# Kernel tuning notes

Measured on AMD Instinct MI355X. Metric: run time of the kernel, lower is better.

Reference implementation:

```python
import jax, jax.numpy as jnp
import numpy as np

D_MODEL = 1024
N_HEADS = 16
HEAD_DIM = D_MODEL // N_HEADS
ALPHA = 1.5
SEQ, BATCH = 4096, 8


def reduced_sparsemax(z, alpha):
    # projection of z/alpha onto the simplex along the last axis
    zs = z / alpha
    z_sorted = -jnp.sort(-zs, axis=-1)          # descending sort
    z_cumsum = jnp.cumsum(z_sorted, axis=-1)
    d = zs.shape[-1]
    r = jnp.arange(1, d + 1, dtype=zs.dtype)
    support = (z_sorted - (z_cumsum - 1.0) / r) > 0
    k = jnp.sum(support, axis=-1, keepdims=True)
    k_safe = jnp.clip(k, 1, None)
    tau_sum = jnp.take_along_axis(z_cumsum, k_safe - 1, axis=-1)
    tau = (tau_sum - 1.0) / k_safe.astype(zs.dtype)
    return jnp.clip(zs - tau, 0.0, None)


def setup_inputs() -> dict:
    key = jax.random.key(0)
    ks = jax.random.split(key, 11)
    s = 0.02
    return {
        "query": jax.random.normal(ks[0], (SEQ, BATCH, D_MODEL), jnp.float32),
        "key":   jax.random.normal(ks[1], (SEQ, BATCH, D_MODEL), jnp.float32),
        "value": jax.random.normal(ks[2], (SEQ, BATCH, D_MODEL), jnp.float32),
        "Wq": jax.random.normal(ks[3], (D_MODEL, D_MODEL), jnp.float32) * s,
        "bq": jnp.zeros((D_MODEL,), jnp.float32),
        "Wk": jax.random.normal(ks[4], (D_MODEL, D_MODEL), jnp.float32) * s,
        "bk": jnp.zeros((D_MODEL,), jnp.float32),
        "Wv": jax.random.normal(ks[5], (D_MODEL, D_MODEL), jnp.float32) * s,
        "bv": jnp.zeros((D_MODEL,), jnp.float32),
        "Wo": jax.random.normal(ks[6], (D_MODEL, D_MODEL), jnp.float32) * s,
        "bo": jnp.zeros((D_MODEL,), jnp.float32),
    }


def reference(query, key, value, Wq, bq, Wk, bk, Wv, bv, Wo, bo):
    A, B, D = query.shape  # (seq, batch, d_model) per the torch code's indexing
    H, hd = N_HEADS, HEAD_DIM
    Q = query @ Wq.T + bq
    K = key @ Wk.T + bk
    V = value @ Wv.T + bv
    # view(A, B, H, hd).transpose(0, 1) -> (B, A, H, hd)
    Q = jnp.swapaxes(Q.reshape(A, B, H, hd), 0, 1)
    K = jnp.swapaxes(K.reshape(A, B, H, hd), 0, 1)
    V = jnp.swapaxes(V.reshape(A, B, H, hd), 0, 1)
    # NOTE: faithful to the original code, attention is across HEADS:
    # scores shape (B, A, H, H)
    scores = jnp.einsum('bahd,bagd->bahg', Q, K) / jnp.sqrt(
        jnp.asarray(hd, jnp.float32))
    attn = reduced_sparsemax(scores, ALPHA)
    attn_out = jnp.einsum('bahg,bagd->bahd', attn, V)  # (B, A, H, hd)
    # transpose(1,2).view(B, -1, D): (B, H, A, hd) flattened to (B, A, D)
    attn_out = jnp.swapaxes(attn_out, 1, 2).reshape(B, -1, D)
    out = attn_out @ Wo.T + bo           # (B, A, D)
    return jnp.swapaxes(out, 0, 1)       # (A, B, D)
```

## Files before the change

### kernel.cpp

```cpp
#include <hip/hip_runtime.h>
#include <hip/hip_bf16.h>
#include <stdint.h>

typedef __bf16 bf16_t;
typedef __bf16 bf16x4 __attribute__((ext_vector_type(4)));
typedef __bf16 bf16x8 __attribute__((ext_vector_type(8)));
typedef float  f32x4  __attribute__((ext_vector_type(4)));

#define AS_G __attribute__((address_space(1)))
#define AS_L __attribute__((address_space(3)))

__global__ void cast_f32_bf16(const float* __restrict__ src, bf16_t* __restrict__ dst) {
    int i = blockIdx.x * 256 + threadIdx.x;
    float4 v = ((const float4*)src)[i];
    bf16x4 o;
    o.x = (bf16_t)v.x; o.y = (bf16_t)v.y; o.z = (bf16_t)v.z; o.w = (bf16_t)v.w;
    ((bf16x4*)dst)[i] = o;
}

template<int OUT_BF16>
__global__ __launch_bounds__(512, 2)
void gemm_bt_kernel(const bf16_t* __restrict__ A,
                    const bf16_t* __restrict__ Bt,
                    const float* __restrict__ bias,
                    void* __restrict__ Cout,
                    int M, int N, int K) {
    __shared__ bf16_t smem[4][2][256 * 32];

    const int tid  = threadIdx.x;
    const int wave = tid >> 6, lane = tid & 63;
    const int quad = lane >> 4, r16 = lane & 15;
    const int wr = wave >> 2, wc = wave & 3;

    const int nbx = N >> 8;
    const int cpx = gridDim.x >> 3;
    const int swz = (blockIdx.x & 7) * cpx + (blockIdx.x >> 3);
    const int m0 = (swz / nbx) << 8;
    const int n0 = (swz % nbx) << 8;

    const int c0 = tid, c1 = 512 + tid;
    const int r0 = c0 >> 2, cc0 = c0 & 3;
    const int r1 = c1 >> 2, cc1 = c1 & 3;
    const int s0 = (r0 & 3) ^ ((r0 >> 2) & 3);
    const int s1 = (r1 & 3) ^ ((r1 >> 2) & 3);
    const bf16_t* gA0 = A  + (size_t)(m0 + r0) * K + ((cc0 ^ s0) << 3);
    const bf16_t* gA1 = A  + (size_t)(m0 + r1) * K + ((cc1 ^ s1) << 3);
    const bf16_t* gB0 = Bt + (size_t)(n0 + r0) * K + ((cc0 ^ s0) << 3);
    const bf16_t* gB1 = Bt + (size_t)(n0 + r1) * K + ((cc1 ^ s1) << 3);

#define STAGE(bufi, kt) do {                                                                    \
        const int _ko = (kt) << 5;                                                              \
        __builtin_amdgcn_global_load_lds((AS_G void*)(gA0 + _ko), (AS_L void*)(&smem[bufi][0][c0 * 8]), 16, 0, 0); \
        __builtin_amdgcn_global_load_lds((AS_G void*)(gA1 + _ko), (AS_L void*)(&smem[bufi][0][c1 * 8]), 16, 0, 0); \
        __builtin_amdgcn_global_load_lds((AS_G void*)(gB0 + _ko), (AS_L void*)(&smem[bufi][1][c0 * 8]), 16, 0, 0); \
        __builtin_amdgcn_global_load_lds((AS_G void*)(gB1 + _ko), (AS_L void*)(&smem[bufi][1][c1 * 8]), 16, 0, 0); \
    } while (0)

    f32x4 acc[8][4] = {};
    const int NT = K >> 5;

    STAGE(0, 0); STAGE(1, 1); STAGE(2, 2);

    const int swzc = quad ^ (r16 & 3) ^ ((r16 >> 2) & 3);
    const int aoff = ((wr * 128 + r16) << 5) + (swzc << 3);
    const int boff = ((wc * 64  + r16) << 5) + (swzc << 3);

    for (int t = 0; t < NT; ++t) {
        asm volatile("s_waitcnt vmcnt(8)\n\ts_barrier" ::: "memory");

        if (t + 3 < NT) STAGE((t + 3) & 3, t + 3);

        const bf16_t* pA = &smem[t & 3][0][0];
        const bf16_t* pB = &smem[t & 3][1][0];
        bf16x8 aF[8], bF[4];
#pragma unroll
        for (int i = 0; i < 8; ++i) aF[i] = *(const bf16x8*)(pA + aoff + i * 512);
#pragma unroll
        for (int i = 0; i < 4; ++i) bF[i] = *(const bf16x8*)(pB + boff + i * 512);

        __builtin_amdgcn_s_setprio(1);
#pragma unroll
        for (int tm = 0; tm < 8; ++tm)
#pragma unroll
            for (int tn = 0; tn < 4; ++tn)
                acc[tm][tn] = __builtin_amdgcn_mfma_f32_16x16x32_bf16(aF[tm], bF[tn], acc[tm][tn], 0, 0, 0);
        __builtin_amdgcn_s_setprio(0);
    }
#undef STAGE

    float bv[4];
#pragma unroll
    for (int tn = 0; tn < 4; ++tn) bv[tn] = bias[n0 + wc * 64 + tn * 16 + r16];

#pragma unroll
    for (int tm = 0; tm < 8; ++tm) {
#pragma unroll
        for (int r = 0; r < 4; ++r) {
            const int m = m0 + wr * 128 + tm * 16 + quad * 4 + r;
#pragma unroll
            for (int tn = 0; tn < 4; ++tn) {
                const int n = n0 + wc * 64 + tn * 16 + r16;
                const float v = acc[tm][tn][r] + bv[tn];
                if (OUT_BF16) ((bf16_t*)Cout)[(size_t)m * N + n] = (bf16_t)v;
                else          ((float*)Cout)[(size_t)m * N + n]  = v;
            }
        }
    }
}

__global__ void attn_kernel(const bf16_t* __restrict__ Q, const bf16_t* __restrict__ K,
                            const bf16_t* __restrict__ V, bf16_t* __restrict__ M2) {
    __shared__ float zs_s[4][16][17];
    __shared__ float tau_s[4][16];
    const int wave = threadIdx.x >> 6, lane = threadIdx.x & 63;
    const int quad = lane >> 4, g16 = lane & 15;
    const int p = blockIdx.x * 4 + wave;
    const int a = p >> 3, b = p & 7;
    const bf16_t* q = Q + (size_t)p * 1024;
    const bf16_t* k = K + (size_t)p * 1024;
    const bf16_t* v = V + (size_t)p * 1024;

    bf16x8 qa0 = *(const bf16x8*)(q + g16 * 64 + quad * 8);
    bf16x8 qa1 = *(const bf16x8*)(q + g16 * 64 + 32 + quad * 8);
    bf16x8 ka0 = *(const bf16x8*)(k + g16 * 64 + quad * 8);
    bf16x8 ka1 = *(const bf16x8*)(k + g16 * 64 + 32 + quad * 8);
    f32x4 sc = {0.f, 0.f, 0.f, 0.f};
    sc = __builtin_amdgcn_mfma_f32_16x16x32_bf16(qa0, ka0, sc, 0, 0, 0);
    sc = __builtin_amdgcn_mfma_f32_16x16x32_bf16(qa1, ka1, sc, 0, 0, 0);

    const float inv = 1.0f / 12.0f;
#pragma unroll
    for (int r = 0; r < 4; ++r) zs_s[wave][quad * 4 + r][g16] = sc[r] * inv;
    __syncthreads();

    if (lane < 16) {
        float z[16];
#pragma unroll
        for (int j = 0; j < 16; ++j) z[j] = zs_s[wave][lane][j];
#pragma unroll
        for (int kk = 2; kk <= 16; kk <<= 1) {
#pragma unroll
            for (int j = kk >> 1; j > 0; j >>= 1) {
#pragma unroll
                for (int i = 0; i < 16; ++i) {
                    int ixj = i ^ j;
                    if (ixj > i) {
                        bool desc = ((i & kk) == 0);
                        float zi = z[i], zj = z[ixj];
                        bool sw = desc ? (zi < zj) : (zi > zj);
                        z[i]   = sw ? zj : zi;
                        z[ixj] = sw ? zi : zj;
                    }
                }
            }
        }
        float cum = 0.f, csel = 0.f;
        int ksel = 1;
#pragma unroll
        for (int j = 0; j < 16; ++j) {
            cum += z[j];
            bool sup = z[j] * (float)(j + 1) > (cum - 1.0f);
            ksel = sup ? (j + 1) : ksel;
            csel = sup ? cum : csel;
        }
        tau_s[wave][lane] = (csel - 1.0f) / (float)ksel;
    }
    __syncthreads();

#pragma unroll
    for (int r = 0; r < 4; ++r) {
        float av = sc[r] * inv - tau_s[wave][quad * 4 + r];
        zs_s[wave][quad * 4 + r][g16] = av > 0.f ? av : 0.f;
    }
    __syncthreads();

    bf16x8 aP;
#pragma unroll
    for (int j = 0; j < 8; ++j) {
        float f = (quad < 2) ? zs_s[wave][g16][quad * 8 + j] : 0.f;
        aP[j] = (bf16_t)f;
    }
#pragma unroll
    for (int c = 0; c < 4; ++c) {
        bf16x8 bV;
#pragma unroll
        for (int j = 0; j < 8; ++j) {
            int g = quad * 8 + j;
            bV[j] = (quad < 2) ? v[g * 64 + c * 16 + g16] : (bf16_t)0.f;
        }
        f32x4 oc = {0.f, 0.f, 0.f, 0.f};
        oc = __builtin_amdgcn_mfma_f32_16x16x32_bf16(aP, bV, oc, 0, 0, 0);
#pragma unroll
        for (int r = 0; r < 4; ++r) {
            int h = quad * 4 + r;
            int e = c * 16 + g16;
            int rr = (h << 8) + (a >> 4);
            int c2 = ((a & 15) << 6) + e;
            M2[((size_t)(rr * 8 + b)) * 1024 + c2] = (bf16_t)oc[r];
        }
    }
}

extern "C" void kernel_launch(void* const* d_in, const int* in_sizes, int n_in,
                              void* d_out, int out_size, void* d_ws, size_t ws_size,
                              hipStream_t stream) {
    (void)in_sizes; (void)n_in; (void)out_size; (void)ws_size;
    const float* query = (const float*)d_in[0];
    const float* key   = (const float*)d_in[1];
    const float* value = (const float*)d_in[2];
    const float* Wq = (const float*)d_in[3];
    const float* bq = (const float*)d_in[4];
    const float* Wk = (const float*)d_in[5];
    const float* bk = (const float*)d_in[6];
    const float* Wv = (const float*)d_in[7];
    const float* bv = (const float*)d_in[8];
    const float* Wo = (const float*)d_in[9];
    const float* bo = (const float*)d_in[10];

    const int M = 32768, D = 1024;
    const size_t MD = (size_t)M * D;

    uint8_t* ws = (uint8_t*)d_ws;
    bf16_t* abuf = (bf16_t*)ws;
    bf16_t* Qb   = (bf16_t*)(ws + MD * 2);
    bf16_t* Kb   = Qb + MD;
    bf16_t* Vb   = Kb + MD;
    bf16_t* M2   = Vb + MD;
    bf16_t* Wqb  = M2 + MD;
    bf16_t* Wkb  = Wqb + (size_t)D * D;
    bf16_t* Wvb  = Wkb + (size_t)D * D;
    bf16_t* Wob  = Wvb + (size_t)D * D;

    const int wBlocks = D * D / 1024;
    const int aBlocks = (int)(MD / 1024);
    cast_f32_bf16<<<wBlocks, 256, 0, stream>>>(Wq, Wqb);
    cast_f32_bf16<<<wBlocks, 256, 0, stream>>>(Wk, Wkb);
    cast_f32_bf16<<<wBlocks, 256, 0, stream>>>(Wv, Wvb);
    cast_f32_bf16<<<wBlocks, 256, 0, stream>>>(Wo, Wob);

    const int gblk = (M / 256) * (D / 256);

    cast_f32_bf16<<<aBlocks, 256, 0, stream>>>(query, abuf);
    gemm_bt_kernel<1><<<gblk, 512, 0, stream>>>(abuf, Wqb, bq, Qb, M, D, D);
    cast_f32_bf16<<<aBlocks, 256, 0, stream>>>(key, abuf);
    gemm_bt_kernel<1><<<gblk, 512, 0, stream>>>(abuf, Wkb, bk, Kb, M, D, D);
    cast_f32_bf16<<<aBlocks, 256, 0, stream>>>(value, abuf);
    gemm_bt_kernel<1><<<gblk, 512, 0, stream>>>(abuf, Wvb, bv, Vb, M, D, D);

    attn_kernel<<<M / 4, 256, 0, stream>>>(Qb, Kb, Vb, M2);

    gemm_bt_kernel<0><<<gblk, 512, 0, stream>>>(M2, Wob, bo, (float*)d_out, M, D, D);
}
```

Measured before the change: 795.6 us.

## Double-buffer BK=64 GEMM tiles with interleaved LDS reads and MFMA phases

Changes the GEMM main loop from a 4-stage pipeline with K-tile 32 to a 2-stage pipeline with K-tile 64. It uses a new 8-column XOR swizzle and splits each iteration into four LDS-read plus MFMA sub-phases separated by sched_barriers. The goal is fewer barriers per unit of K and better overlap of LDS fragment loads with MFMA issue. The cost is shallower prefetch depth, which can expose global-load latency, plus an extra barrier per iteration to guard buffer reuse.

```diff
diff --git a/kernel.cpp b/kernel.cpp
--- a/kernel.cpp
+++ b/kernel.cpp
@@ -25,7 +25,7 @@
                     const float* __restrict__ bias,
                     void* __restrict__ Cout,
                     int M, int N, int K) {
-    __shared__ bf16_t smem[4][2][256 * 32];
+    __shared__ bf16_t smem[2][2][256 * 64];
 
     const int tid  = threadIdx.x;
     const int wave = tid >> 6, lane = tid & 63;
@@ -38,53 +38,104 @@
     const int m0 = (swz / nbx) << 8;
     const int n0 = (swz % nbx) << 8;
 
-    const int c0 = tid, c1 = 512 + tid;
-    const int r0 = c0 >> 2, cc0 = c0 & 3;
-    const int r1 = c1 >> 2, cc1 = c1 & 3;
-    const int s0 = (r0 & 3) ^ ((r0 >> 2) & 3);
-    const int s1 = (r1 & 3) ^ ((r1 >> 2) & 3);
-    const bf16_t* gA0 = A  + (size_t)(m0 + r0) * K + ((cc0 ^ s0) << 3);
-    const bf16_t* gA1 = A  + (size_t)(m0 + r1) * K + ((cc1 ^ s1) << 3);
-    const bf16_t* gB0 = Bt + (size_t)(n0 + r0) * K + ((cc0 ^ s0) << 3);
-    const bf16_t* gB1 = Bt + (size_t)(n0 + r1) * K + ((cc1 ^ s1) << 3);
-
-#define STAGE(bufi, kt) do {                                                                    \
-        const int _ko = (kt) << 5;                                                              \
-        __builtin_amdgcn_global_load_lds((AS_G void*)(gA0 + _ko), (AS_L void*)(&smem[bufi][0][c0 * 8]), 16, 0, 0); \
-        __builtin_amdgcn_global_load_lds((AS_G void*)(gA1 + _ko), (AS_L void*)(&smem[bufi][0][c1 * 8]), 16, 0, 0); \
-        __builtin_amdgcn_global_load_lds((AS_G void*)(gB0 + _ko), (AS_L void*)(&smem[bufi][1][c0 * 8]), 16, 0, 0); \
-        __builtin_amdgcn_global_load_lds((AS_G void*)(gB1 + _ko), (AS_L void*)(&smem[bufi][1][c1 * 8]), 16, 0, 0); \
+    const int cc[4] = { tid, tid + 512, tid + 1024, tid + 1536 };
+    const bf16_t* gA[4]; const bf16_t* gB[4];
+#pragma unroll
+    for (int u = 0; u < 4; ++u) {
+        const int row = cc[u] >> 3;
+        const int kc  = (cc[u] & 7) ^ (row & 7);
+        gA[u] = A  + (size_t)(m0 + row) * K + (kc << 3);
+        gB[u] = Bt + (size_t)(n0 + row) * K + (kc << 3);
+    }
+
+#define STAGE(bufi, kt) do {                                                                      \
+        const int _ko = (kt) << 6;                                                                \
+        __builtin_amdgcn_global_load_lds((AS_G void*)(gA[0] + _ko), (AS_L void*)(&smem[bufi][0][cc[0] * 8]), 16, 0, 0); \
+        __builtin_amdgcn_global_load_lds((AS_G void*)(gA[1] + _ko), (AS_L void*)(&smem[bufi][0][cc[1] * 8]), 16, 0, 0); \
+        __builtin_amdgcn_global_load_lds((AS_G void*)(gA[2] + _ko), (AS_L void*)(&smem[bufi][0][cc[2] * 8]), 16, 0, 0); \
+        __builtin_amdgcn_global_load_lds((AS_G void*)(gA[3] + _ko), (AS_L void*)(&smem[bufi][0][cc[3] * 8]), 16, 0, 0); \
+        __builtin_amdgcn_global_load_lds((AS_G void*)(gB[0] + _ko), (AS_L void*)(&smem[bufi][1][cc[0] * 8]), 16, 0, 0); \
+        __builtin_amdgcn_global_load_lds((AS_G void*)(gB[1] + _ko), (AS_L void*)(&smem[bufi][1][cc[1] * 8]), 16, 0, 0); \
+        __builtin_amdgcn_global_load_lds((AS_G void*)(gB[2] + _ko), (AS_L void*)(&smem[bufi][1][cc[2] * 8]), 16, 0, 0); \
+        __builtin_amdgcn_global_load_lds((AS_G void*)(gB[3] + _ko), (AS_L void*)(&smem[bufi][1][cc[3] * 8]), 16, 0, 0); \
     } while (0)
 
+    const int arow = wr * 128 + r16;
+    const int brow = wc * 64  + r16;
+    const int sw0 = (0 | quad) ^ (r16 & 7);
+    const int sw1 = (4 | quad) ^ (r16 & 7);
+    const int aoff0 = arow * 64 + sw0 * 8, aoff1 = arow * 64 + sw1 * 8;
+    const int boff0 = brow * 64 + sw0 * 8, boff1 = brow * 64 + sw1 * 8;
+
     f32x4 acc[8][4] = {};
-    const int NT = K >> 5;
-
-    STAGE(0, 0); STAGE(1, 1); STAGE(2, 2);
-
-    const int swzc = quad ^ (r16 & 3) ^ ((r16 >> 2) & 3);
-    const int aoff = ((wr * 128 + r16) << 5) + (swzc << 3);
-    const int boff = ((wc * 64  + r16) << 5) + (swzc << 3);
+    const int NT = K >> 6;
+
+    STAGE(0, 0);
 
     for (int t = 0; t < NT; ++t) {
-        asm volatile("s_waitcnt vmcnt(8)\n\ts_barrier" ::: "memory");
-
-        if (t + 3 < NT) STAGE((t + 3) & 3, t + 3);
-
-        const bf16_t* pA = &smem[t & 3][0][0];
-        const bf16_t* pB = &smem[t & 3][1][0];
-        bf16x8 aF[8], bF[4];
-#pragma unroll
-        for (int i = 0; i < 8; ++i) aF[i] = *(const bf16x8*)(pA + aoff + i * 512);
-#pragma unroll
-        for (int i = 0; i < 4; ++i) bF[i] = *(const bf16x8*)(pB + boff + i * 512);
-
+        if (t + 1 < NT) {
+            STAGE((t + 1) & 1, t + 1);
+            asm volatile("s_waitcnt vmcnt(8)" ::: "memory");
+        } else {
+            asm volatile("s_waitcnt vmcnt(0)" ::: "memory");
+        }
+        __builtin_amdgcn_s_barrier();
+        __builtin_amdgcn_sched_barrier(0);
+
+        const bf16_t* pA = &smem[t & 1][0][0];
+        const bf16_t* pB = &smem[t & 1][1][0];
+        bf16x8 b0[4], a0[4], a1[4], b1[4], a2[4], a3[4];
+
+#pragma unroll
+        for (int i = 0; i < 4; ++i) b0[i] = *(const bf16x8*)(pB + boff0 + i * 1024);
+#pragma unroll
+        for (int i = 0; i < 4; ++i) a0[i] = *(const bf16x8*)(pA + aoff0 + i * 1024);
         __builtin_amdgcn_s_setprio(1);
 #pragma unroll
-        for (int tm = 0; tm < 8; ++tm)
+        for (int tm = 0; tm < 4; ++tm)
 #pragma unroll
             for (int tn = 0; tn < 4; ++tn)
-                acc[tm][tn] = __builtin_amdgcn_mfma_f32_16x16x32_bf16(aF[tm], bF[tn], acc[tm][tn], 0, 0, 0);
+                acc[tm][tn] = __builtin_amdgcn_mfma_f32_16x16x32_bf16(a0[tm], b0[tn], acc[tm][tn], 0, 0, 0);
         __builtin_amdgcn_s_setprio(0);
+        __builtin_amdgcn_sched_barrier(0);
+
+#pragma unroll
+        for (int i = 0; i < 4; ++i) a1[i] = *(const bf16x8*)(pA + aoff0 + (4 + i) * 1024);
+        __builtin_amdgcn_s_setprio(1);
+#pragma unroll
+        for (int tm = 0; tm < 4; ++tm)
+#pragma unroll
+            for (int tn = 0; tn < 4; ++tn)
+                acc[4 + tm][tn] = __builtin_amdgcn_mfma_f32_16x16x32_bf16(a1[tm], b0[tn], acc[4 + tm][tn], 0, 0, 0);
+        __builtin_amdgcn_s_setprio(0);
+        __builtin_amdgcn_sched_barrier(0);
+
+#pragma unroll
+        for (int i = 0; i < 4; ++i) b1[i] = *(const bf16x8*)(pB + boff1 + i * 1024);
+#pragma unroll
+        for (int i = 0; i < 4; ++i) a2[i] = *(const bf16x8*)(pA + aoff1 + i * 1024);
+        __builtin_amdgcn_s_setprio(1);
+#pragma unroll
+        for (int tm = 0; tm < 4; ++tm)
+#pragma unroll
+            for (int tn = 0; tn < 4; ++tn)
+                acc[tm][tn] = __builtin_amdgcn_mfma_f32_16x16x32_bf16(a2[tm], b1[tn], acc[tm][tn], 0, 0, 0);
+        __builtin_amdgcn_s_setprio(0);
+        __builtin_amdgcn_sched_barrier(0);
+
+#pragma unroll
+        for (int i = 0; i < 4; ++i) a3[i] = *(const bf16x8*)(pA + aoff1 + (4 + i) * 1024);
+        __builtin_amdgcn_s_setprio(1);
+#pragma unroll
+        for (int tm = 0; tm < 4; ++tm)
+#pragma unroll
+            for (int tn = 0; tn < 4; ++tn)
+                acc[4 + tm][tn] = __builtin_amdgcn_mfma_f32_16x16x32_bf16(a3[tm], b1[tn], acc[4 + tm][tn], 0, 0, 0);
+        __builtin_amdgcn_s_setprio(0);
+        __builtin_amdgcn_sched_barrier(0);
+
+        __builtin_amdgcn_s_barrier();
+        __builtin_amdgcn_sched_barrier(0);
     }
 #undef STAGE
 
```

Result: no change. 783.7 us (-1.5%).
